# Performance work log

Hardware: AMD Instinct MI355X
Metric: run time of the kernel (lower is better)

## Reference

```python
import jax, jax.numpy as jnp
import numpy as np

B, L, H = 8, 2048, 1024
Q_END = 63  # question_ends


def setup_inputs() -> dict:
    key = jax.random.key(0)
    k1, k2 = jax.random.split(key)
    encoder_out = jax.random.normal(k1, (B, L, H), dtype=jnp.float32)
    # simW: nn.Linear(3H, 1, bias=False) -> weight vector of length 3H
    w = jax.random.normal(k2, (3 * H,), dtype=jnp.float32) * (1.0 / np.sqrt(3 * H))
    return {"encoder_out": encoder_out, "w": w, "question_ends": Q_END}


def reference(encoder_out, w, question_ends):
    h = encoder_out.shape[-1]
    j_len = question_ends + 1  # static python int
    query = encoder_out[:, :j_len, :]    # (B, J, H)
    context = encoder_out[:, j_len:, :]  # (B, T, H)
    # Decompose simW(cat(c, q, c*q)) = c.w_c + q.w_q + sum_h c_h q_h w_m_h
    w_c, w_q, w_m = w[:h], w[h:2 * h], w[2 * h:]
    c_term = context @ w_c               # (B, T)
    q_term = query @ w_q                 # (B, J)
    cross = jnp.einsum('bth,bjh->btj', context * w_m, query)  # (B, T, J)
    S = c_term[:, :, None] + q_term[:, None, :] + cross        # (B, T, J)
    # context-to-query attention
    c2q = jnp.einsum('btj,bjh->bth', jax.nn.softmax(S, axis=-1), query)  # (B, T, H)
    # query-to-context attention
    b_att = jax.nn.softmax(jnp.max(S, axis=2), axis=-1)  # (B, T)
    q2c = jnp.einsum('bt,bth->bh', b_att, context)[:, None, :]  # (B, 1, H), broadcasts over T
    G = jnp.concatenate(
        [context, c2q, context * c2q, context * q2c], axis=-1)  # (B, T, 4H)
    return (query, G)
```

## Files before the change

kernel.cpp:

```cpp
#include <hip/hip_runtime.h>
#include <math.h>

#define BB 8
#define LL 2048
#define HH 1024
#define JL 64
#define TT 1984
#define NT 31

#define QT_OFF   0
#define PQ_OFF   (QT_OFF + BB*JL)
#define PDEN_OFF (PQ_OFF + BB*NT*HH)
#define PMAX_OFF (PDEN_OFF + 256)
#define Q2C_OFF  (PMAX_OFF + 256)
#define QTR_OFF  (Q2C_OFF + BB*HH)
#define PWS_OFF  (QTR_OFF + BB*HH*JL/2)

typedef __attribute__((ext_vector_type(8))) short bf16x8;
typedef __attribute__((ext_vector_type(4))) float f32x4;

__device__ inline ushort f2bf(float x) {
  uint u = __float_as_uint(x);
  return (ushort)((u + 0x7FFFu + ((u >> 16) & 1u)) >> 16);
}

__device__ inline void nt_store4(float* p, float a, float b2, float c, float d) {
  f32x4 v = {a, b2, c, d};
  __builtin_nontemporal_store(v, (f32x4*)p);
}

__global__ __launch_bounds__(256) void k0(const float* __restrict__ enc,
                                          const float* __restrict__ w,
                                          float* __restrict__ out,
                                          float* __restrict__ ws) {
  int j = blockIdx.x, b = blockIdx.y, tid = threadIdx.x;
  const float* qrow = enc + ((size_t)b*LL + j)*HH;
  float4 v = *(const float4*)(qrow + tid*4);
  *(float4*)(out + ((size_t)b*JL + j)*HH + tid*4) = v;
  ushort* qT = (ushort*)(ws + QTR_OFF) + (size_t)b*HH*JL + j;
  qT[(size_t)(tid*4+0)*JL] = f2bf(v.x);
  qT[(size_t)(tid*4+1)*JL] = f2bf(v.y);
  qT[(size_t)(tid*4+2)*JL] = f2bf(v.z);
  qT[(size_t)(tid*4+3)*JL] = f2bf(v.w);
  float4 wq = *(const float4*)(w + HH + tid*4);
  float a = v.x*wq.x + v.y*wq.y + v.z*wq.z + v.w*wq.w;
  #pragma unroll
  for (int o = 32; o > 0; o >>= 1) a += __shfl_xor(a, o);
  __shared__ float red[4];
  if ((tid & 63) == 0) red[tid >> 6] = a;
  __syncthreads();
  if (tid == 0) ws[QT_OFF + b*JL + j] = red[0]+red[1]+red[2]+red[3];
}

__global__ __launch_bounds__(256) void kA(const float* __restrict__ enc,
                                          const float* __restrict__ w,
                                          float* __restrict__ ws) {
  __shared__ ushort ctx_s[64][72];
  __shared__ ushort qm_s[64][72];
  __shared__ ushort P_s[64][72];
  __shared__ float m_s[64];
  __shared__ float w_s[64];
  const int b = blockIdx.y, bx = blockIdx.x;
  const int t0 = bx * 64;
  const int tid = threadIdx.x;
  const int lane = tid & 63, wv = tid >> 6;
  const int fr = lane & 15, fg = lane >> 4;
  const float* ctx = enc + ((size_t)b*LL + JL)*HH;
  const float* qry = enc + (size_t)b*LL*HH;
  const float* wc = w;
  const float* wm = w + 2*HH;
  f32x4 acc[4];
  #pragma unroll
  for (int n = 0; n < 4; ++n) acc[n] = (f32x4){0.f,0.f,0.f,0.f};
  const int sr = tid >> 2;
  const int sc = (tid & 3) * 16;
  for (int h0 = 0; h0 < HH; h0 += 64) {
    #pragma unroll
    for (int q = 0; q < 4; ++q) {
      const int hc = h0 + sc + q*4;
      float4 cv = *(const float4*)(ctx + (size_t)(t0 + sr)*HH + hc);
      float4 qv = *(const float4*)(qry + (size_t)sr*HH + hc);
      float4 mv = *(const float4*)(wm + hc);
      float4 wvv = *(const float4*)(wc + hc);
      ushort4 cb = make_ushort4(f2bf(cv.x), f2bf(cv.y), f2bf(cv.z), f2bf(cv.w));
      ushort4 qb = make_ushort4(f2bf(qv.x*mv.x + wvv.x), f2bf(qv.y*mv.y + wvv.y),
                                f2bf(qv.z*mv.z + wvv.z), f2bf(qv.w*mv.w + wvv.w));
      *(ushort4*)&ctx_s[sr][sc + q*4] = cb;
      *(ushort4*)&qm_s[sr][sc + q*4] = qb;
    }
    __syncthreads();
    #pragma unroll
    for (int kk = 0; kk < 2; ++kk) {
      bf16x8 a = *(const bf16x8*)&ctx_s[wv*16 + fr][kk*32 + fg*8];
      #pragma unroll
      for (int n = 0; n < 4; ++n) {
        bf16x8 bb = *(const bf16x8*)&qm_s[n*16 + fr][kk*32 + fg*8];
        acc[n] = __builtin_amdgcn_mfma_f32_16x16x32_bf16(a, bb, acc[n], 0, 0, 0);
      }
    }
    __syncthreads();
  }
  float qt[4];
  #pragma unroll
  for (int n = 0; n < 4; ++n) qt[n] = ws[QT_OFF + (size_t)b*JL + n*16 + fr];
  #pragma unroll
  for (int r = 0; r < 4; ++r) {
    float s0 = acc[0][r] + qt[0];
    float s1 = acc[1][r] + qt[1];
    float s2 = acc[2][r] + qt[2];
    float s3 = acc[3][r] + qt[3];
    float m = fmaxf(fmaxf(s0,s1), fmaxf(s2,s3));
    #pragma unroll
    for (int o = 1; o < 16; o <<= 1) m = fmaxf(m, __shfl_xor(m, o));
    float e0 = __expf(s0-m), e1 = __expf(s1-m), e2 = __expf(s2-m), e3 = __expf(s3-m);
    float sum = e0+e1+e2+e3;
    #pragma unroll
    for (int o = 1; o < 16; o <<= 1) sum += __shfl_xor(sum, o);
    float inv = 1.f/sum;
    const int row = wv*16 + fg*4 + r;
    if (fr == 0) m_s[row] = m;
    P_s[row][ 0 + fr] = f2bf(e0*inv);
    P_s[row][16 + fr] = f2bf(e1*inv);
    P_s[row][32 + fr] = f2bf(e2*inv);
    P_s[row][48 + fr] = f2bf(e3*inv);
  }
  __syncthreads();
  if (tid < 64) {
    float mv2 = m_s[tid];
    float M = mv2;
    #pragma unroll
    for (int o = 1; o < 64; o <<= 1) M = fmaxf(M, __shfl_xor(M, o));
    float wv2 = __expf(mv2 - M);
    w_s[tid] = wv2;
    float den = wv2;
    #pragma unroll
    for (int o = 1; o < 64; o <<= 1) den += __shfl_xor(den, o);
    if (tid == 0) {
      ws[PDEN_OFF + b*NT + bx] = den;
      ws[PMAX_OFF + b*NT + bx] = M;
    }
  }
  __syncthreads();
  ushort* Pb = (ushort*)(ws + PWS_OFF) + ((size_t)b*TT + t0)*JL;
  #pragma unroll
  for (int q = 0; q < 2; ++q) {
    int idx = q*256 + tid;
    int row = idx >> 3, g = idx & 7;
    *(uint4*)(Pb + (size_t)row*JL + g*8) = *(const uint4*)&P_s[row][g*8];
  }
  {
    const int hc = tid * 4;
    const float* ctxb = ctx + (size_t)t0*HH + hc;
    float4 a0 = {0,0,0,0}, a1 = {0,0,0,0};
    #pragma unroll 8
    for (int t = 0; t < 64; t += 2) {
      float w0 = w_s[t], w1 = w_s[t+1];
      float4 v0 = *(const float4*)(ctxb + (size_t)t*HH);
      float4 v1 = *(const float4*)(ctxb + (size_t)(t+1)*HH);
      a0.x += w0*v0.x; a0.y += w0*v0.y; a0.z += w0*v0.z; a0.w += w0*v0.w;
      a1.x += w1*v1.x; a1.y += w1*v1.y; a1.z += w1*v1.z; a1.w += w1*v1.w;
    }
    a0.x += a1.x; a0.y += a1.y; a0.z += a1.z; a0.w += a1.w;
    *(float4*)(ws + PQ_OFF + ((size_t)(b*NT + bx))*HH + hc) = a0;
  }
}

__global__ __launch_bounds__(256) void k2(float* __restrict__ ws) {
  int b = blockIdx.x, tid = threadIdx.x;
  float M = -1e30f;
  #pragma unroll
  for (int c = 0; c < NT; ++c) M = fmaxf(M, ws[PMAX_OFF + b*NT + c]);
  float den = 0.f;
  #pragma unroll
  for (int c = 0; c < NT; ++c)
    den += __expf(ws[PMAX_OFF + b*NT + c] - M) * ws[PDEN_OFF + b*NT + c];
  float inv = 1.f / den;
  float4 a = {0,0,0,0};
  for (int c = 0; c < NT; ++c) {
    float e = __expf(ws[PMAX_OFF + b*NT + c] - M);
    float4 v = *(const float4*)(ws + PQ_OFF + ((size_t)(b*NT + c))*HH + tid*4);
    a.x += e*v.x; a.y += e*v.y; a.z += e*v.z; a.w += e*v.w;
  }
  a.x *= inv; a.y *= inv; a.z *= inv; a.w *= inv;
  *(float4*)(ws + Q2C_OFF + (size_t)b*HH + tid*4) = a;
}

__global__ __launch_bounds__(256) void kB(const float* __restrict__ enc,
                                          const float* __restrict__ ws,
                                          float* __restrict__ out) {
  __shared__ ushort P_s[16][72];
  __shared__ float c2q_s[16][260];
  const int b = blockIdx.y, t0 = blockIdx.x*16, tid = threadIdx.x;
  const int lane = tid & 63, wv = tid >> 6;
  const int fr = lane & 15, fg = lane >> 4;
  const ushort* Pb = (const ushort*)(ws + PWS_OFF) + ((size_t)b*TT + t0)*JL;
  if (tid < 128) {
    int row = tid >> 3, g = tid & 7;
    *(uint4*)&P_s[row][g*8] = *(const uint4*)(Pb + (size_t)row*JL + g*8);
  }
  const ushort* qTg = (const ushort*)(ws + QTR_OFF) + (size_t)b*HH*JL;
  const float* ctx = enc + ((size_t)b*LL + JL)*HH;
  float* G = out + (size_t)BB*JL*HH + (size_t)b*TT*4096;
  __syncthreads();
  for (int h0 = 0; h0 < HH; h0 += 256) {
    f32x4 acc2[4];
    #pragma unroll
    for (int hh = 0; hh < 4; ++hh) acc2[hh] = (f32x4){0.f,0.f,0.f,0.f};
    #pragma unroll
    for (int hh = 0; hh < 4; ++hh) {
      #pragma unroll
      for (int kk = 0; kk < 2; ++kk) {
        bf16x8 a = *(const bf16x8*)(qTg + (size_t)(h0 + wv*64 + hh*16 + fr)*JL + kk*32 + fg*8);
        bf16x8 bb = *(const bf16x8*)&P_s[fr][kk*32 + fg*8];
        acc2[hh] = __builtin_amdgcn_mfma_f32_16x16x32_bf16(a, bb, acc2[hh], 0, 0, 0);
      }
    }
    #pragma unroll
    for (int hh = 0; hh < 4; ++hh)
      *(f32x4*)&c2q_s[fr][wv*64 + hh*16 + fg*4] = acc2[hh];
    __syncthreads();
    {
      const int hl = lane * 4;
      float4 qc = *(const float4*)(ws + Q2C_OFF + (size_t)b*HH + h0 + hl);
      #pragma unroll
      for (int p = 0; p < 4; ++p) {
        const int t = p*4 + wv;
        float4 c2 = *(const float4*)&c2q_s[t][hl];
        float4 cv = *(const float4*)(ctx + (size_t)(t0 + t)*HH + h0 + hl);
        float* Gr = G + (size_t)(t0 + t)*4096 + h0 + hl;
        nt_store4(Gr,        cv.x, cv.y, cv.z, cv.w);
        nt_store4(Gr + 1024, c2.x, c2.y, c2.z, c2.w);
        nt_store4(Gr + 2048, cv.x*c2.x, cv.y*c2.y, cv.z*c2.z, cv.w*c2.w);
        nt_store4(Gr + 3072, cv.x*qc.x, cv.y*qc.y, cv.z*qc.z, cv.w*qc.w);
      }
    }
    __syncthreads();
  }
}

extern "C" void kernel_launch(void* const* d_in, const int* in_sizes, int n_in,
                              void* d_out, int out_size, void* d_ws, size_t ws_size,
                              hipStream_t stream) {
  const float* enc = (const float*)d_in[0];
  const float* w   = (const float*)d_in[1];
  float* out = (float*)d_out;
  float* ws  = (float*)d_ws;
  k0<<<dim3(JL, BB), 256, 0, stream>>>(enc, w, out, ws);
  kA<<<dim3(NT, BB), 256, 0, stream>>>(enc, w, ws);
  k2<<<BB, 256, 0, stream>>>(ws);
  kB<<<dim3(TT/16, BB), 256, 0, stream>>>(enc, ws, out);
}
```

Baseline: 114.7 us.

## Halve kA tile to 32 rows and double-buffer c2q in kB

kA now processes 32 context rows per block instead of 64, doubling the grid to 62x8 blocks. The four waves split the 64 query columns into two halves, so the row softmax needs cross-wave max/sum reductions through shared memory with extra barriers. kB prefetches context rows and q2c into registers before the MFMA step and double-buffers the c2q shared tile, which removes one barrier per chunk. The aim is better CU occupancy for kA (previously 248 blocks) and overlap of loads with compute in kB, at the cost of reloading the query tile twice as often and more partial results for k2 to reduce.

```diff
diff --git a/kernel.cpp b/kernel.cpp
--- a/kernel.cpp
+++ b/kernel.cpp
@@ -6,13 +6,13 @@
 #define HH 1024
 #define JL 64
 #define TT 1984
-#define NT 31
+#define NT2 62
 
 #define QT_OFF   0
 #define PQ_OFF   (QT_OFF + BB*JL)
-#define PDEN_OFF (PQ_OFF + BB*NT*HH)
-#define PMAX_OFF (PDEN_OFF + 256)
-#define Q2C_OFF  (PMAX_OFF + 256)
+#define PDEN_OFF (PQ_OFF + BB*NT2*HH)
+#define PMAX_OFF (PDEN_OFF + 512)
+#define Q2C_OFF  (PMAX_OFF + 512)
 #define QTR_OFF  (Q2C_OFF + BB*HH)
 #define PWS_OFF  (QTR_OFF + BB*HH*JL/2)
 
@@ -55,97 +55,113 @@
 __global__ __launch_bounds__(256) void kA(const float* __restrict__ enc,
                                           const float* __restrict__ w,
                                           float* __restrict__ ws) {
-  __shared__ ushort ctx_s[64][72];
+  __shared__ ushort ctx_s[32][72];
   __shared__ ushort qm_s[64][72];
-  __shared__ ushort P_s[64][72];
-  __shared__ float m_s[64];
-  __shared__ float w_s[64];
+  __shared__ ushort P_s[32][72];
+  __shared__ float mpart[32][2];
+  __shared__ float spart[32][2];
+  __shared__ float m_s[32];
+  __shared__ float w_s[32];
   const int b = blockIdx.y, bx = blockIdx.x;
-  const int t0 = bx * 64;
+  const int t0 = bx * 32;
   const int tid = threadIdx.x;
-  const int lane = tid & 63, wv = tid >> 6;
+  const int lane = tid & 63, wvi = tid >> 6;
   const int fr = lane & 15, fg = lane >> 4;
+  const int mrow = (wvi & 1) * 16;
+  const int nhalf = wvi >> 1;
   const float* ctx = enc + ((size_t)b*LL + JL)*HH;
   const float* qry = enc + (size_t)b*LL*HH;
   const float* wc = w;
   const float* wm = w + 2*HH;
-  f32x4 acc[4];
-  #pragma unroll
-  for (int n = 0; n < 4; ++n) acc[n] = (f32x4){0.f,0.f,0.f,0.f};
-  const int sr = tid >> 2;
-  const int sc = (tid & 3) * 16;
+  f32x4 acc[2];
+  acc[0] = (f32x4){0.f,0.f,0.f,0.f};
+  acc[1] = (f32x4){0.f,0.f,0.f,0.f};
   for (int h0 = 0; h0 < HH; h0 += 64) {
     #pragma unroll
-    for (int q = 0; q < 4; ++q) {
-      const int hc = h0 + sc + q*4;
-      float4 cv = *(const float4*)(ctx + (size_t)(t0 + sr)*HH + hc);
-      float4 qv = *(const float4*)(qry + (size_t)sr*HH + hc);
-      float4 mv = *(const float4*)(wm + hc);
-      float4 wvv = *(const float4*)(wc + hc);
-      ushort4 cb = make_ushort4(f2bf(cv.x), f2bf(cv.y), f2bf(cv.z), f2bf(cv.w));
-      ushort4 qb = make_ushort4(f2bf(qv.x*mv.x + wvv.x), f2bf(qv.y*mv.y + wvv.y),
-                                f2bf(qv.z*mv.z + wvv.z), f2bf(qv.w*mv.w + wvv.w));
-      *(ushort4*)&ctx_s[sr][sc + q*4] = cb;
-      *(ushort4*)&qm_s[sr][sc + q*4] = qb;
+    for (int it = 0; it < 2; ++it) {
+      int idx = it*256 + tid;
+      int r = idx >> 4, c4 = idx & 15;
+      float4 cv = *(const float4*)(ctx + (size_t)(t0 + r)*HH + h0 + c4*4);
+      *(ushort4*)&ctx_s[r][c4*4] =
+          make_ushort4(f2bf(cv.x), f2bf(cv.y), f2bf(cv.z), f2bf(cv.w));
+    }
+    #pragma unroll
+    for (int it = 0; it < 4; ++it) {
+      int idx = it*256 + tid;
+      int r = idx >> 4, c4 = idx & 15;
+      float4 qv = *(const float4*)(qry + (size_t)r*HH + h0 + c4*4);
+      float4 mv = *(const float4*)(wm + h0 + c4*4);
+      float4 wvv = *(const float4*)(wc + h0 + c4*4);
+      *(ushort4*)&qm_s[r][c4*4] =
+          make_ushort4(f2bf(qv.x*mv.x + wvv.x), f2bf(qv.y*mv.y + wvv.y),
+                       f2bf(qv.z*mv.z + wvv.z), f2bf(qv.w*mv.w + wvv.w));
     }
     __syncthreads();
     #pragma unroll
     for (int kk = 0; kk < 2; ++kk) {
-      bf16x8 a = *(const bf16x8*)&ctx_s[wv*16 + fr][kk*32 + fg*8];
+      bf16x8 a = *(const bf16x8*)&ctx_s[mrow + fr][kk*32 + fg*8];
       #pragma unroll
-      for (int n = 0; n < 4; ++n) {
-        bf16x8 bb = *(const bf16x8*)&qm_s[n*16 + fr][kk*32 + fg*8];
-        acc[n] = __builtin_amdgcn_mfma_f32_16x16x32_bf16(a, bb, acc[n], 0, 0, 0);
+      for (int nf = 0; nf < 2; ++nf) {
+        bf16x8 bb = *(const bf16x8*)&qm_s[nhalf*32 + nf*16 + fr][kk*32 + fg*8];
+        acc[nf] = __builtin_amdgcn_mfma_f32_16x16x32_bf16(a, bb, acc[nf], 0, 0, 0);
       }
     }
     __syncthreads();
   }
-  float qt[4];
-  #pragma unroll
-  for (int n = 0; n < 4; ++n) qt[n] = ws[QT_OFF + (size_t)b*JL + n*16 + fr];
+  float qt0 = ws[QT_OFF + (size_t)b*JL + nhalf*32 + fr];
+  float qt1 = ws[QT_OFF + (size_t)b*JL + nhalf*32 + 16 + fr];
+  float s0r[4], s1r[4], e0r[4], e1r[4], mr[4];
   #pragma unroll
   for (int r = 0; r < 4; ++r) {
-    float s0 = acc[0][r] + qt[0];
-    float s1 = acc[1][r] + qt[1];
-    float s2 = acc[2][r] + qt[2];
-    float s3 = acc[3][r] + qt[3];
-    float m = fmaxf(fmaxf(s0,s1), fmaxf(s2,s3));
-    #pragma unroll
-    for (int o = 1; o < 16; o <<= 1) m = fmaxf(m, __shfl_xor(m, o));
-    float e0 = __expf(s0-m), e1 = __expf(s1-m), e2 = __expf(s2-m), e3 = __expf(s3-m);
-    float sum = e0+e1+e2+e3;
-    #pragma unroll
-    for (int o = 1; o < 16; o <<= 1) sum += __shfl_xor(sum, o);
-    float inv = 1.f/sum;
-    const int row = wv*16 + fg*4 + r;
-    if (fr == 0) m_s[row] = m;
-    P_s[row][ 0 + fr] = f2bf(e0*inv);
-    P_s[row][16 + fr] = f2bf(e1*inv);
-    P_s[row][32 + fr] = f2bf(e2*inv);
-    P_s[row][48 + fr] = f2bf(e3*inv);
-  }
-  __syncthreads();
-  if (tid < 64) {
+    s0r[r] = acc[0][r] + qt0;
+    s1r[r] = acc[1][r] + qt1;
+    float pm = fmaxf(s0r[r], s1r[r]);
+    #pragma unroll
+    for (int o = 1; o < 16; o <<= 1) pm = fmaxf(pm, __shfl_xor(pm, o));
+    if (fr == 0) mpart[mrow + fg*4 + r][nhalf] = pm;
+  }
+  __syncthreads();
+  #pragma unroll
+  for (int r = 0; r < 4; ++r) {
+    const int row = mrow + fg*4 + r;
+    float m = fmaxf(mpart[row][0], mpart[row][1]);
+    mr[r] = m;
+    e0r[r] = __expf(s0r[r] - m);
+    e1r[r] = __expf(s1r[r] - m);
+    float ps = e0r[r] + e1r[r];
+    #pragma unroll
+    for (int o = 1; o < 16; o <<= 1) ps += __shfl_xor(ps, o);
+    if (fr == 0) spart[row][nhalf] = ps;
+  }
+  __syncthreads();
+  #pragma unroll
+  for (int r = 0; r < 4; ++r) {
+    const int row = mrow + fg*4 + r;
+    float inv = 1.f / (spart[row][0] + spart[row][1]);
+    P_s[row][nhalf*32 +      fr] = f2bf(e0r[r]*inv);
+    P_s[row][nhalf*32 + 16 + fr] = f2bf(e1r[r]*inv);
+    if (fr == 0 && nhalf == 0) m_s[row] = mr[r];
+  }
+  __syncthreads();
+  if (tid < 32) {
     float mv2 = m_s[tid];
     float M = mv2;
     #pragma unroll
-    for (int o = 1; o < 64; o <<= 1) M = fmaxf(M, __shfl_xor(M, o));
+    for (int o = 1; o < 32; o <<= 1) M = fmaxf(M, __shfl_xor(M, o));
     float wv2 = __expf(mv2 - M);
     w_s[tid] = wv2;
     float den = wv2;
     #pragma unroll
-    for (int o = 1; o < 64; o <<= 1) den += __shfl_xor(den, o);
+    for (int o = 1; o < 32; o <<= 1) den += __shfl_xor(den, o);
     if (tid == 0) {
-      ws[PDEN_OFF + b*NT + bx] = den;
-      ws[PMAX_OFF + b*NT + bx] = M;
-    }
-  }
-  __syncthreads();
-  ushort* Pb = (ushort*)(ws + PWS_OFF) + ((size_t)b*TT + t0)*JL;
-  #pragma unroll
-  for (int q = 0; q < 2; ++q) {
-    int idx = q*256 + tid;
-    int row = idx >> 3, g = idx & 7;
+      ws[PDEN_OFF + b*NT2 + bx] = den;
+      ws[PMAX_OFF + b*NT2 + bx] = M;
+    }
+  }
+  __syncthreads();
+  {
+    ushort* Pb = (ushort*)(ws + PWS_OFF) + ((size_t)b*TT + t0)*JL;
+    int row = tid >> 3, g = tid & 7;
     *(uint4*)(Pb + (size_t)row*JL + g*8) = *(const uint4*)&P_s[row][g*8];
   }
   {
@@ -153,7 +169,7 @@
     const float* ctxb = ctx + (size_t)t0*HH + hc;
     float4 a0 = {0,0,0,0}, a1 = {0,0,0,0};
     #pragma unroll 8
-    for (int t = 0; t < 64; t += 2) {
+    for (int t = 0; t < 32; t += 2) {
       float w0 = w_s[t], w1 = w_s[t+1];
       float4 v0 = *(const float4*)(ctxb + (size_t)t*HH);
       float4 v1 = *(const float4*)(ctxb + (size_t)(t+1)*HH);
@@ -161,7 +177,7 @@
       a1.x += w1*v1.x; a1.y += w1*v1.y; a1.z += w1*v1.z; a1.w += w1*v1.w;
     }
     a0.x += a1.x; a0.y += a1.y; a0.z += a1.z; a0.w += a1.w;
-    *(float4*)(ws + PQ_OFF + ((size_t)(b*NT + bx))*HH + hc) = a0;
+    *(float4*)(ws + PQ_OFF + ((size_t)(b*NT2 + bx))*HH + hc) = a0;
   }
 }
 
@@ -169,16 +185,16 @@
   int b = blockIdx.x, tid = threadIdx.x;
   float M = -1e30f;
   #pragma unroll
-  for (int c = 0; c < NT; ++c) M = fmaxf(M, ws[PMAX_OFF + b*NT + c]);
+  for (int c = 0; c < NT2; ++c) M = fmaxf(M, ws[PMAX_OFF + b*NT2 + c]);
   float den = 0.f;
   #pragma unroll
-  for (int c = 0; c < NT; ++c)
-    den += __expf(ws[PMAX_OFF + b*NT + c] - M) * ws[PDEN_OFF + b*NT + c];
+  for (int c = 0; c < NT2; ++c)
+    den += __expf(ws[PMAX_OFF + b*NT2 + c] - M) * ws[PDEN_OFF + b*NT2 + c];
   float inv = 1.f / den;
   float4 a = {0,0,0,0};
-  for (int c = 0; c < NT; ++c) {
-    float e = __expf(ws[PMAX_OFF + b*NT + c] - M);
-    float4 v = *(const float4*)(ws + PQ_OFF + ((size_t)(b*NT + c))*HH + tid*4);
+  for (int c = 0; c < NT2; ++c) {
+    float e = __expf(ws[PMAX_OFF + b*NT2 + c] - M);
+    float4 v = *(const float4*)(ws + PQ_OFF + ((size_t)(b*NT2 + c))*HH + tid*4);
     a.x += e*v.x; a.y += e*v.y; a.z += e*v.z; a.w += e*v.w;
   }
   a.x *= inv; a.y *= inv; a.z *= inv; a.w *= inv;
@@ -189,9 +205,9 @@
                                           const float* __restrict__ ws,
                                           float* __restrict__ out) {
   __shared__ ushort P_s[16][72];
-  __shared__ float c2q_s[16][260];
+  __shared__ float c2q_s[2][16][260];
   const int b = blockIdx.y, t0 = blockIdx.x*16, tid = threadIdx.x;
-  const int lane = tid & 63, wv = tid >> 6;
+  const int lane = tid & 63, wvi = tid >> 6;
   const int fr = lane & 15, fg = lane >> 4;
   const ushort* Pb = (const ushort*)(ws + PWS_OFF) + ((size_t)b*TT + t0)*JL;
   if (tid < 128) {
@@ -201,8 +217,16 @@
   const ushort* qTg = (const ushort*)(ws + QTR_OFF) + (size_t)b*HH*JL;
   const float* ctx = enc + ((size_t)b*LL + JL)*HH;
   float* G = out + (size_t)BB*JL*HH + (size_t)b*TT*4096;
-  __syncthreads();
-  for (int h0 = 0; h0 < HH; h0 += 256) {
+  const int hl = lane * 4;
+  __syncthreads();
+  for (int ch = 0; ch < 4; ++ch) {
+    const int h0 = ch * 256;
+    const int cur = ch & 1;
+    float4 ctxr[4];
+    #pragma unroll
+    for (int p = 0; p < 4; ++p)
+      ctxr[p] = *(const float4*)(ctx + (size_t)(t0 + p*4 + wvi)*HH + h0 + hl);
+    float4 qcr = *(const float4*)(ws + Q2C_OFF + (size_t)b*HH + h0 + hl);
     f32x4 acc2[4];
     #pragma unroll
     for (int hh = 0; hh < 4; ++hh) acc2[hh] = (f32x4){0.f,0.f,0.f,0.f};
@@ -210,31 +234,26 @@
     for (int hh = 0; hh < 4; ++hh) {
       #pragma unroll
       for (int kk = 0; kk < 2; ++kk) {
-        bf16x8 a = *(const bf16x8*)(qTg + (size_t)(h0 + wv*64 + hh*16 + fr)*JL + kk*32 + fg*8);
+        bf16x8 a = *(const bf16x8*)(qTg + (size_t)(h0 + wvi*64 + hh*16 + fr)*JL + kk*32 + fg*8);
         bf16x8 bb = *(const bf16x8*)&P_s[fr][kk*32 + fg*8];
         acc2[hh] = __builtin_amdgcn_mfma_f32_16x16x32_bf16(a, bb, acc2[hh], 0, 0, 0);
       }
     }
     #pragma unroll
     for (int hh = 0; hh < 4; ++hh)
-      *(f32x4*)&c2q_s[fr][wv*64 + hh*16 + fg*4] = acc2[hh];
+      *(f32x4*)&c2q_s[cur][fr][wvi*64 + hh*16 + fg*4] = acc2[hh];
     __syncthreads();
-    {
-      const int hl = lane * 4;
-      float4 qc = *(const float4*)(ws + Q2C_OFF + (size_t)b*HH + h0 + hl);
-      #pragma unroll
-      for (int p = 0; p < 4; ++p) {
-        const int t = p*4 + wv;
-        float4 c2 = *(const float4*)&c2q_s[t][hl];
-        float4 cv = *(const float4*)(ctx + (size_t)(t0 + t)*HH + h0 + hl);
-        float* Gr = G + (size_t)(t0 + t)*4096 + h0 + hl;
-        nt_store4(Gr,        cv.x, cv.y, cv.z, cv.w);
-        nt_store4(Gr + 1024, c2.x, c2.y, c2.z, c2.w);
-        nt_store4(Gr + 2048, cv.x*c2.x, cv.y*c2.y, cv.z*c2.z, cv.w*c2.w);
-        nt_store4(Gr + 3072, cv.x*qc.x, cv.y*qc.y, cv.z*qc.z, cv.w*qc.w);
-      }
-    }
-    __syncthreads();
+    #pragma unroll
+    for (int p = 0; p < 4; ++p) {
+      const int t = p*4 + wvi;
+      float4 c2 = *(const float4*)&c2q_s[cur][t][hl];
+      float4 cv = ctxr[p];
+      float* Gr = G + (size_t)(t0 + t)*4096 + h0 + hl;
+      nt_store4(Gr,        cv.x, cv.y, cv.z, cv.w);
+      nt_store4(Gr + 1024, c2.x, c2.y, c2.z, c2.w);
+      nt_store4(Gr + 2048, cv.x*c2.x, cv.y*c2.y, cv.z*c2.z, cv.w*c2.w);
+      nt_store4(Gr + 3072, cv.x*qcr.x, cv.y*qcr.y, cv.z*qcr.z, cv.w*qcr.w);
+    }
   }
 }
 
@@ -246,7 +265,7 @@
   float* out = (float*)d_out;
   float* ws  = (float*)d_ws;
   k0<<<dim3(JL, BB), 256, 0, stream>>>(enc, w, out, ws);
-  kA<<<dim3(NT, BB), 256, 0, stream>>>(enc, w, ws);
+  kA<<<dim3(NT2, BB), 256, 0, stream>>>(enc, w, ws);
   k2<<<BB, 256, 0, stream>>>(ws);
   kB<<<dim3(TT/16, BB), 256, 0, stream>>>(enc, ws, out);
 }
```

New measurement: 110.4 us. -3.7%, faster.
